# Optimization experiments

Hardware: AMD Instinct MI355X
Metric: run time of the kernel (lower is better)

Reference implementation:

```python
import jax, jax.numpy as jnp
import numpy as np

G, D, O, L, H, K, B = 33538, 256, 512, 6, 8, 2048, 4
FF = 4 * D
EPS = 1e-5
THRESH = 0.0


def _ln(x, s, b):
    mu = jnp.mean(x, axis=-1, keepdims=True)
    var = jnp.mean((x - mu) ** 2, axis=-1, keepdims=True)
    return (x - mu) * jax.lax.rsqrt(var + EPS) * s + b


def setup_inputs() -> dict:
    key = jax.random.key(0)
    ks = iter(jax.random.split(key, 32))
    s = 0.02
    rn = lambda shape, scale=s: jax.random.normal(next(ks), shape, dtype=jnp.float32) * scale
    inp = {
        'expr': jax.random.normal(next(ks), (B, G), dtype=jnp.float32),
        'gene_emb': rn((G, D)),
        'ep_w1': rn((D, 1), 0.5), 'ep_b1': jnp.zeros((D,), jnp.float32),
        'ep_w2': rn((D, D)), 'ep_b2': jnp.zeros((D,), jnp.float32),
        'cls': rn((D,), 1.0),
        'ln1_s': jnp.ones((L, D), jnp.float32), 'ln1_b': jnp.zeros((L, D), jnp.float32),
        'qkv_w': rn((L, 3 * D, D)), 'qkv_b': jnp.zeros((L, 3 * D), jnp.float32),
        'out_w': rn((L, D, D)), 'out_b': jnp.zeros((L, D), jnp.float32),
        'ln2_s': jnp.ones((L, D), jnp.float32), 'ln2_b': jnp.zeros((L, D), jnp.float32),
        'ff_w1': rn((L, FF, D)), 'ff_b1': jnp.zeros((L, FF), jnp.float32),
        'ff_w2': rn((L, D, FF)), 'ff_b2': jnp.zeros((L, D), jnp.float32),
        'fn_s': jnp.ones((D,), jnp.float32), 'fn_b': jnp.zeros((D,), jnp.float32),
        'pr_w1': rn((O, D)), 'pr_b1': jnp.zeros((O,), jnp.float32),
        'pr_w2': rn((O, O)), 'pr_b2': jnp.zeros((O,), jnp.float32),
    }
    return inp


def _encoder(expr, gene_emb, ep_w1, ep_b1, ep_w2, ep_b2, cls,
             ln1_s, ln1_b, qkv_w, qkv_b, out_w, out_b, ln2_s, ln2_b,
             ff_w1, ff_b1, ff_w2, ff_b2, fn_s, fn_b,
             pr_w1, pr_b1, pr_w2, pr_b2):
    Bb, Gg = expr.shape
    # --- tokeniser: token_i = gene_emb[i] + MLP(expr_i) for all genes ---
    h = jax.nn.gelu(expr[..., None] * ep_w1[:, 0] + ep_b1, approximate=False)  # [B,G,D]
    val_emb = jnp.einsum('bgd,ed->bge', h, ep_w2) + ep_b2
    tokens_all = gene_emb[None] + val_emb  # [B,G,D]
    # active-gene selection: threshold AND top-K
    active = expr > THRESH
    _, topk_idx = jax.lax.top_k(expr, K)
    sel = jnp.zeros((Bb, Gg), bool).at[jnp.arange(Bb)[:, None], topk_idx].set(True)
    active = active & sel
    counts = jnp.sum(active, axis=1)  # [B]
    # vectorized ragged packing: stable sort puts active genes (ascending id) first
    order = jnp.argsort(jnp.logical_not(active), axis=1, stable=True)[:, :K]  # [B,K]
    gathered = jnp.take_along_axis(tokens_all, order[..., None], axis=1)      # [B,K,D]
    valid = jnp.arange(K)[None, :] < counts[:, None]                          # [B,K]
    body = jnp.where(valid[..., None], gathered, 0.0)
    tokens = jnp.concatenate([jnp.broadcast_to(cls, (Bb, 1, D)), body], axis=1)  # [B,T,D]
    mask = jnp.concatenate([jnp.ones((Bb, 1), bool), valid], axis=1)             # [B,T]
    T = K + 1
    dh = D // H
    bias = jnp.where(mask, 0.0, -1e9)[:, None, None, :]  # key padding
    x = tokens
    for i in range(L):
        y = _ln(x, ln1_s[i], ln1_b[i])
        qkv = y @ qkv_w[i].T + qkv_b[i]
        q, k, v = jnp.split(qkv, 3, axis=-1)
        q = q.reshape(Bb, T, H, dh).transpose(0, 2, 1, 3)
        k = k.reshape(Bb, T, H, dh).transpose(0, 2, 1, 3)
        v = v.reshape(Bb, T, H, dh).transpose(0, 2, 1, 3)
        scores = jnp.einsum('bhqd,bhkd->bhqk', q, k) / np.sqrt(dh) + bias
        a = jax.nn.softmax(scores, axis=-1)
        o = jnp.einsum('bhqk,bhkd->bhqd', a, v).transpose(0, 2, 1, 3).reshape(Bb, T, D)
        x = x + o @ out_w[i].T + out_b[i]
        y2 = _ln(x, ln2_s[i], ln2_b[i])
        x = x + jax.nn.gelu(y2 @ ff_w1[i].T + ff_b1[i], approximate=False) @ ff_w2[i].T + ff_b2[i]
    x = _ln(x, fn_s, fn_b)
    cls_out = x[:, 0]
    return jax.nn.gelu(cls_out @ pr_w1.T + pr_b1, approximate=False) @ pr_w2.T + pr_b2


def reference(expr, gene_emb, ep_w1, ep_b1, ep_w2, ep_b2, cls,
              ln1_s, ln1_b, qkv_w, qkv_b, out_w, out_b, ln2_s, ln2_b,
              ff_w1, ff_b1, ff_w2, ff_b2, fn_s, fn_b,
              pr_w1, pr_b1, pr_w2, pr_b2):
    return _encoder(expr, gene_emb, ep_w1, ep_b1, ep_w2, ep_b2, cls,
                    ln1_s, ln1_b, qkv_w, qkv_b, out_w, out_b, ln2_s, ln2_b,
                    ff_w1, ff_b1, ff_w2, ff_b2, fn_s, fn_b,
                    pr_w1, pr_b1, pr_w2, pr_b2)
```

## Files before the change

### kernel.cpp

```cpp
#include <hip/hip_runtime.h>
#include <hip/hip_bf16.h>
#include <math.h>

#define GG 33538
#define DD 256
#define LL 6
#define HH 8
#define KK 2048
#define BB 4
#define TT 2049
#define BT (BB*TT)
#define NT 65
#define QSC (0.17677669529663688f * 1.44269504088896340f)

typedef __bf16 bf16x8 __attribute__((ext_vector_type(8)));
typedef float f32x4 __attribute__((ext_vector_type(4)));
typedef float f32x16 __attribute__((ext_vector_type(16)));
typedef unsigned short ub16;

union BW { __bf16 h; ub16 u; };
__device__ __forceinline__ ub16 f2b(float x) { BW w; w.h = (__bf16)x; return w.u; }
__device__ __forceinline__ unsigned pk2(float a, float b) {
    return (unsigned)f2b(a) | ((unsigned)f2b(b) << 16);
}
union U4B { unsigned u[4]; bf16x8 v; };

__device__ __forceinline__ float gelu_f(float x) {
    return 0.5f * x * (1.0f + erff(x * 0.70710678118654752440f));
}

__device__ __forceinline__ unsigned to_key(float x) {
    unsigned u = __float_as_uint(x);
    return (u & 0x80000000u) ? ~u : (u | 0x80000000u);
}

__device__ int block_scan_excl_1024(int v, int* shw) {
    int lane = threadIdx.x & 63, w = threadIdx.x >> 6;
    int x = v;
    #pragma unroll
    for (int o = 1; o < 64; o <<= 1) {
        int t = __shfl_up(x, o, 64);
        if (lane >= o) x += t;
    }
    if (lane == 63) shw[w] = x;
    __syncthreads();
    if (w == 0) {
        int y = (lane < 16) ? shw[lane] : 0;
        #pragma unroll
        for (int o = 1; o < 16; o <<= 1) {
            int t = __shfl_up(y, o, 64);
            if (lane >= o) y += t;
        }
        if (lane < 16) shw[lane] = y;
    }
    __syncthreads();
    int off = (w == 0) ? 0 : shw[w - 1];
    return off + x - v;
}

#define TKCH 33

__global__ __launch_bounds__(1024) void topk_kernel(const float* __restrict__ expr,
                                                    int* __restrict__ idxout,
                                                    int* __restrict__ cntout) {
    __shared__ unsigned hist[16][256];
    __shared__ int shw[16];
    __shared__ unsigned sh_prefix;
    __shared__ int sh_want;
    __shared__ int sh_tot2;

    int b = blockIdx.x;
    int tid = threadIdx.x, wv = tid >> 6;
    const float* row = expr + (size_t)b * GG;

    unsigned prefix = 0;
    int want = KK;
    for (int p = 3; p >= 0; --p) {
        for (int i = tid; i < 16 * 256; i += 1024) ((unsigned*)hist)[i] = 0u;
        __syncthreads();
        int shift = p * 8;
        unsigned pmask = (p == 3) ? 0u : (0xFFFFFFFFu << (shift + 8));
        for (int i = tid; i < GG / 4; i += 1024) {
            float4 v4 = *(const float4*)(row + 4 * i);
            float vv[4] = {v4.x, v4.y, v4.z, v4.w};
            #pragma unroll
            for (int j = 0; j < 4; ++j) {
                unsigned key = to_key(vv[j]);
                if ((key & pmask) == (prefix & pmask))
                    atomicAdd(&hist[wv][(key >> shift) & 255u], 1u);
            }
        }
        if (tid < 2) {
            unsigned key = to_key(row[33536 + tid]);
            if ((key & pmask) == (prefix & pmask))
                atomicAdd(&hist[15][(key >> shift) & 255u], 1u);
        }
        __syncthreads();
        unsigned cnt = 0;
        if (tid < 256) {
            #pragma unroll
            for (int j = 1; j < 16; ++j) cnt += hist[j][tid];
            cnt += hist[0][tid];
            hist[0][tid] = cnt;
        }
        __syncthreads();
        int v = (tid < 256) ? (int)hist[0][255 - tid] : 0;
        int above = block_scan_excl_1024(v, shw);
        if (tid < 256 && above < want && above + v >= want) {
            sh_prefix = prefix | ((unsigned)(255 - tid) << shift);
            sh_want = want - above;
        }
        __syncthreads();
        prefix = sh_prefix;
        want = sh_want;
        __syncthreads();
    }
    unsigned kth = prefix;

    int start = tid * TKCH;
    int end = min(start + TKCH, GG);
    int c_eq = 0;
    for (int g = start; g < end; ++g) c_eq += (to_key(row[g]) == kth);
    int eq_base = block_scan_excl_1024(c_eq, shw);

    int c_act = 0;
    {
        int leq = 0;
        for (int g = start; g < end; ++g) {
            float e = row[g];
            unsigned key = to_key(e);
            bool sel = (key > kth) || (key == kth && (eq_base + leq) < want);
            leq += (key == kth);
            c_act += (sel && e > 0.0f) ? 1 : 0;
        }
    }
    int out_base = block_scan_excl_1024(c_act, shw);
    if (tid == 1023) sh_tot2 = out_base + c_act;
    {
        int leq = 0, pos = out_base;
        for (int g = start; g < end; ++g) {
            float e = row[g];
            unsigned key = to_key(e);
            bool sel = (key > kth) || (key == kth && (eq_base + leq) < want);
            leq += (key == kth);
            if (sel && e > 0.0f) idxout[b * KK + pos++] = g;
        }
    }
    __syncthreads();
    if (tid == 0) cntout[b] = sh_tot2;
}

__global__ __launch_bounds__(256) void cvt_bf16_kernel(const float* __restrict__ s,
                                                       ub16* __restrict__ d, int n) {
    int i = blockIdx.x * 256 + threadIdx.x;
    if (i < n) d[i] = f2b(s[i]);
}

__global__ __launch_bounds__(256) void build_h_kernel(const float* __restrict__ expr,
                                                      const int* __restrict__ idxb,
                                                      const int* __restrict__ cntb,
                                                      const float* __restrict__ ep_w1,
                                                      const float* __restrict__ ep_b1,
                                                      ub16* __restrict__ H) {
    int i = blockIdx.x * 256 + threadIdx.x;
    int r = i >> 8, d = i & 255;
    int b = r >> 11, jj = r & (KK - 1);
    float v = 0.0f;
    if (jj < cntb[b]) {
        int g = idxb[b * KK + jj];
        float e = expr[(size_t)b * GG + g];
        v = gelu_f(e * ep_w1[d] + ep_b1[d]);
    }
    H[i] = f2b(v);
}

__global__ __launch_bounds__(256) void assemble_kernel(const float* __restrict__ VAL,
                                                       const float* __restrict__ gene_emb,
                                                       const float* __restrict__ clsv,
                                                       const int* __restrict__ idxb,
                                                       const int* __restrict__ cntb,
                                                       float* __restrict__ x) {
    int i = blockIdx.x * 256 + threadIdx.x;
    int r = i >> 8, d = i & 255;
    int b = r / TT, t = r % TT;
    float v;
    if (t == 0) {
        v = clsv[d];
    } else {
        int jj = t - 1;
        if (jj < cntb[b]) {
            int g = idxb[b * KK + jj];
            v = gene_emb[(size_t)g * DD + d] + VAL[((size_t)b * KK + jj) * DD + d];
        } else {
            v = 0.0f;
        }
    }
    x[i] = v;
}

__global__ __launch_bounds__(256) void ln_kernel(const float* __restrict__ X,
                                                 const float* __restrict__ s,
                                                 const float* __restrict__ bsh,
                                                 ub16* __restrict__ Y16,
                                                 float* __restrict__ Yf) {
    int w = threadIdx.x >> 6, lane = threadIdx.x & 63;
    size_t r = (size_t)blockIdx.x * 4 + w;
    float4 xv = *(const float4*)(X + r * 256 + lane * 4);
    float sum = xv.x + xv.y + xv.z + xv.w;
    #pragma unroll
    for (int o = 1; o < 64; o <<= 1) sum += __shfl_xor(sum, o);
    float mu = sum * (1.0f / 256.0f);
    float d0 = xv.x - mu, d1 = xv.y - mu, d2 = xv.z - mu, d3 = xv.w - mu;
    float vs = d0 * d0 + d1 * d1 + d2 * d2 + d3 * d3;
    #pragma unroll
    for (int o = 1; o < 64; o <<= 1) vs += __shfl_xor(vs, o);
    float rstd = rsqrtf(vs * (1.0f / 256.0f) + 1e-5f);
    float4 sc = *(const float4*)(s + lane * 4);
    float4 bc = *(const float4*)(bsh + lane * 4);
    float y0 = d0 * rstd * sc.x + bc.x;
    float y1 = d1 * rstd * sc.y + bc.y;
    float y2 = d2 * rstd * sc.z + bc.z;
    float y3 = d3 * rstd * sc.w + bc.w;
    if (Y16) {
        uint2 o2 = make_uint2(pk2(y0, y1), pk2(y2, y3));
        *(uint2*)(Y16 + r * 256 + lane * 4) = o2;
    } else {
        *(float4*)(Yf + r * 256 + lane * 4) = make_float4(y0, y1, y2, y3);
    }
}

__global__ __launch_bounds__(256) void gemm_bt16(const ub16* __restrict__ A,
                                                 const ub16* __restrict__ W,
                                                 const float* __restrict__ bias,
                                                 const float* __restrict__ R,
                                                 float* __restrict__ Cf,
                                                 ub16* __restrict__ Ch,
                                                 int M, int N, int K, int gelu_flag,
                                                 int qcols) {
    __shared__ ub16 As[2][64][40];
    __shared__ ub16 Ws[2][64][40];
    int tid = threadIdx.x;
    int lane = tid & 63, w = tid >> 6;
    int wr = (w >> 1) * 32, wc = (w & 1) * 32;
    int bm = blockIdx.y * 64, bn = blockIdx.x * 64;
    f32x4 acc[2][2] = {};

    int lrow = tid >> 2, lc8 = (tid & 3) * 8;
    int arow = min(bm + lrow, M - 1);
    const ub16* ap = A + (size_t)arow * K + lc8;
    const ub16* wp = W + (size_t)(bn + lrow) * K + lc8;

    int fr = lane & 15, fc = 8 * (lane >> 4);
    for (int k0 = 0; k0 < K; k0 += 64) {
        bf16x8 av0 = *(const bf16x8*)(ap + k0);
        bf16x8 av1 = *(const bf16x8*)(ap + k0 + 32);
        bf16x8 wv0 = *(const bf16x8*)(wp + k0);
        bf16x8 wv1 = *(const bf16x8*)(wp + k0 + 32);
        *(bf16x8*)&As[0][lrow][lc8] = av0;
        *(bf16x8*)&As[1][lrow][lc8] = av1;
        *(bf16x8*)&Ws[0][lrow][lc8] = wv0;
        *(bf16x8*)&Ws[1][lrow][lc8] = wv1;
        __syncthreads();
        #pragma unroll
        for (int ks = 0; ks < 2; ++ks) {
            bf16x8 a0 = *(const bf16x8*)&As[ks][wr + fr][fc];
            bf16x8 a1 = *(const bf16x8*)&As[ks][wr + 16 + fr][fc];
            bf16x8 b0 = *(const bf16x8*)&Ws[ks][wc + fr][fc];
            bf16x8 b1 = *(const bf16x8*)&Ws[ks][wc + 16 + fr][fc];
            acc[0][0] = __builtin_amdgcn_mfma_f32_16x16x32_bf16(a0, b0, acc[0][0], 0, 0, 0);
            acc[0][1] = __builtin_amdgcn_mfma_f32_16x16x32_bf16(a0, b1, acc[0][1], 0, 0, 0);
            acc[1][0] = __builtin_amdgcn_mfma_f32_16x16x32_bf16(a1, b0, acc[1][0], 0, 0, 0);
            acc[1][1] = __builtin_amdgcn_mfma_f32_16x16x32_bf16(a1, b1, acc[1][1], 0, 0, 0);
        }
        __syncthreads();
    }

    #pragma unroll
    for (int i = 0; i < 2; ++i) {
        #pragma unroll
        for (int j = 0; j < 2; ++j) {
            #pragma unroll
            for (int reg = 0; reg < 4; ++reg) {
                int gm = bm + wr + i * 16 + (lane >> 4) * 4 + reg;
                int gn = bn + wc + j * 16 + (lane & 15);
                if (gm >= M) continue;
                float v = acc[i][j][reg] + bias[gn];
                if (R) v += R[(size_t)gm * N + gn];
                if (gelu_flag) v = gelu_f(v);
                if (gn < qcols) v *= QSC;
                if (Cf) Cf[(size_t)gm * N + gn] = v;
                else    Ch[(size_t)gm * N + gn] = f2b(v);
            }
        }
    }
}

__global__ __launch_bounds__(256) void kvprep(const ub16* __restrict__ qkv,
                                              ub16* __restrict__ Kc,
                                              ub16* __restrict__ Vt) {
    __shared__ unsigned vl[32][33];
    int bh = blockIdx.x, b = bh >> 3, h = bh & 7;
    int c = blockIdx.y;
    int tid = threadIdx.x;
    int krel = tid >> 2;
    int key = c * 64 + krel;
    int d8 = (tid & 3) * 8;
    U4B kv = {}, vv = {};
    if (key < TT) {
        const ub16* p = qkv + ((size_t)(b * TT + key)) * 768 + 256 + h * 32 + d8;
        kv.v = *(const bf16x8*)p;
        vv.v = *(const bf16x8*)(p + 256);
    }
    int kt = c * 2 + (krel >> 5);
    if (kt < NT)
        *(bf16x8*)(Kc + (((size_t)bh * NT + kt) * 32 + (krel & 31)) * 32 + d8) = kv.v;

    unsigned pu[4];
    #pragma unroll
    for (int j = 0; j < 4; ++j) pu[j] = __shfl_xor(vv.u[j], 4);
    if (!(krel & 1)) {
        int kp = krel >> 1;
        #pragma unroll
        for (int j = 0; j < 8; ++j) {
            unsigned mine = (vv.u[j >> 1] >> ((j & 1) * 16)) & 0xffffu;
            unsigned oth  = (pu[j >> 1] >> ((j & 1) * 16)) & 0xffffu;
            vl[d8 + j][kp] = mine | (oth << 16);
        }
    }
    __syncthreads();
    int d = tid >> 3, c8 = tid & 7;
    int kt2 = c * 2 + (c8 >> 2);
    if (kt2 < NT) {
        unsigned* vdst = (unsigned*)(Vt + (((size_t)bh * NT + kt2) * 32 + d) * 32);
        #pragma unroll
        for (int ih = 0; ih < 2; ++ih) {
            int pkr = (c8 & 3) * 4 + ih * 2;
            int dp = (pkr & 1) | ((pkr & 2) << 1) | ((pkr & 4) >> 1) | (pkr & 8);
            uint2 o2 = make_uint2(vl[d][c8 * 4 + ih * 2], vl[d][c8 * 4 + ih * 2 + 1]);
            *(uint2*)(vdst + dp) = o2;
        }
    }
}

__global__ __launch_bounds__(256) void attn_mfma4(const ub16* __restrict__ qkv,
                                                  const ub16* __restrict__ Kc,
                                                  const ub16* __restrict__ Vt,
                                                  const int* __restrict__ cnt,
                                                  ub16* __restrict__ attno) {
    __shared__ float Olds[4][32][33];
    __shared__ float Oll[4][32];
    int bh = blockIdx.x, b = bh >> 3, h = bh & 7;
    int tid = threadIdx.x;
    int w = tid >> 6, lane = tid & 63, hi = lane >> 5, q = lane & 31;
    int qt = blockIdx.y;
    int t = qt * 32 + q;
    int nvalid = cnt[b] + 1;
    int nkt = (nvalid + 31) >> 5;
    int nfull = (nvalid & 31) ? nkt - 1 : nkt;

    int tc = min(t, TT - 1);
    const ub16* qp = qkv + ((size_t)(b * TT + tc)) * 768 + h * 32 + 8 * hi;
    bf16x8 bq0 = *(const bf16x8*)qp;
    bf16x8 bq1 = *(const bf16x8*)(qp + 16);

    float l = 0.0f;
    f32x16 ot = {};

    const ub16* kp = Kc + ((size_t)bh * NT + w) * 1024 + q * 32 + 8 * hi;
    const ub16* vp = Vt + ((size_t)bh * NT + w) * 1024 + q * 32 + 8 * hi;
    bf16x8 ka0 = *(const bf16x8*)kp;
    bf16x8 ka1 = *(const bf16x8*)(kp + 16);
    bf16x8 va0 = *(const bf16x8*)vp;
    bf16x8 va1 = *(const bf16x8*)(vp + 16);

    for (int kt = w; kt < nkt; kt += 4) {
        bf16x8 nk0 = ka0, nk1 = ka1, nv0 = va0, nv1 = va1;
        if (kt + 4 < nkt) {
            kp += 4096; vp += 4096;
            nk0 = *(const bf16x8*)kp;
            nk1 = *(const bf16x8*)(kp + 16);
            nv0 = *(const bf16x8*)vp;
            nv1 = *(const bf16x8*)(vp + 16);
        }
        f32x16 zz = {};
        f32x16 st = __builtin_amdgcn_mfma_f32_32x32x16_bf16(ka0, bq0, zz, 0, 0, 0);
        st = __builtin_amdgcn_mfma_f32_32x32x16_bf16(ka1, bq1, st, 0, 0, 0);

        if (kt >= nfull) {
            int k0 = kt << 5;
            #pragma unroll
            for (int r = 0; r < 16; ++r) {
                int key = k0 + (r & 3) + 8 * (r >> 2) + 4 * hi;
                if (key >= nvalid) st[r] = -1e30f;
            }
        }
        float tsum = 0.0f;
        #pragma unroll
        for (int r = 0; r < 16; ++r) {
            float p = exp2f(st[r]);
            st[r] = p;
            tsum += p;
        }
        tsum += __shfl_xor(tsum, 32);
        l += tsum;

        U4B p0, p1;
        #pragma unroll
        for (int jj = 0; jj < 4; ++jj) {
            p0.u[jj] = pk2(st[2 * jj], st[2 * jj + 1]);
            p1.u[jj] = pk2(st[8 + 2 * jj], st[9 + 2 * jj]);
        }
        ot = __builtin_amdgcn_mfma_f32_32x32x16_bf16(va0, p0.v, ot, 0, 0, 0);
        ot = __builtin_amdgcn_mfma_f32_32x32x16_bf16(va1, p1.v, ot, 0, 0, 0);

        ka0 = nk0; ka1 = nk1; va0 = nv0; va1 = nv1;
    }

    #pragma unroll
    for (int r = 0; r < 16; ++r) {
        int d = (r & 3) + 8 * (r >> 2) + 4 * hi;
        Olds[w][q][d] = ot[r];
    }
    if (hi == 0) Oll[w][q] = l;
    __syncthreads();

    int qq = tid >> 3, dg = tid & 7;
    int trow = qt * 32 + qq;
    if (trow < TT) {
        float L = Oll[0][qq] + Oll[1][qq] + Oll[2][qq] + Oll[3][qq];
        float rL = 1.0f / L;
        float o[4];
        #pragma unroll
        for (int j = 0; j < 4; ++j) {
            int d = dg * 4 + j;
            o[j] = (Olds[0][qq][d] + Olds[1][qq][d] +
                    Olds[2][qq][d] + Olds[3][qq][d]) * rL;
        }
        uint2 o2 = make_uint2(pk2(o[0], o[1]), pk2(o[2], o[3]));
        *(uint2*)(attno + ((size_t)(b * TT + trow)) * 256 + h * 32 + dg * 4) = o2;
    }
}

__global__ __launch_bounds__(512) void head_kernel(const float* __restrict__ Y,
                                                   const float* __restrict__ w1,
                                                   const float* __restrict__ b1,
                                                   const float* __restrict__ w2,
                                                   const float* __restrict__ b2,
                                                   float* __restrict__ out) {
    __shared__ float clsr[256];
    __shared__ float t1[512];
    int b = blockIdx.x, tid = threadIdx.x;
    if (tid < 256) clsr[tid] = Y[((size_t)b * TT) * DD + tid];
    __syncthreads();
    float acc = b1[tid];
    const float* w = w1 + (size_t)tid * 256;
    for (int k = 0; k < 256; ++k) acc += clsr[k] * w[k];
    t1[tid] = gelu_f(acc);
    __syncthreads();
    float acc2 = b2[tid];
    const float* wr = w2 + (size_t)tid * 512;
    for (int k = 0; k < 512; ++k) acc2 += t1[k] * wr[k];
    out[(size_t)b * 512 + tid] = acc2;
}

extern "C" void kernel_launch(void* const* d_in, const int* in_sizes, int n_in,
                              void* d_out, int out_size, void* d_ws, size_t ws_size,
                              hipStream_t stream) {
    (void)in_sizes; (void)n_in; (void)out_size; (void)ws_size;
    const float* expr     = (const float*)d_in[0];
    const float* gene_emb = (const float*)d_in[1];
    const float* ep_w1    = (const float*)d_in[2];
    const float* ep_b1    = (const float*)d_in[3];
    const float* ep_w2    = (const float*)d_in[4];
    const float* ep_b2    = (const float*)d_in[5];
    const float* clsv     = (const float*)d_in[6];
    const float* ln1_s    = (const float*)d_in[7];
    const float* ln1_b    = (const float*)d_in[8];
    const float* qkv_w    = (const float*)d_in[9];
    const float* qkv_b    = (const float*)d_in[10];
    const float* out_w    = (const float*)d_in[11];
    const float* out_b    = (const float*)d_in[12];
    const float* ln2_s    = (const float*)d_in[13];
    const float* ln2_b    = (const float*)d_in[14];
    const float* ff_w1    = (const float*)d_in[15];
    const float* ff_b1    = (const float*)d_in[16];
    const float* ff_w2    = (const float*)d_in[17];
    const float* ff_b2    = (const float*)d_in[18];
    const float* fn_s     = (const float*)d_in[19];
    const float* fn_b     = (const float*)d_in[20];
    const float* pr_w1    = (const float*)d_in[21];
    const float* pr_b1    = (const float*)d_in[22];
    const float* pr_w2    = (const float*)d_in[23];
    const float* pr_b2    = (const float*)d_in[24];
    float* outp = (float*)d_out;

    const size_t KVSZ = (size_t)32 * NT * 1024;

    float* x   = (float*)d_ws;
    float* VAL = x + (size_t)BT * 256;
    ub16* y16   = (ub16*)(VAL + (size_t)8192 * 256);
    ub16* qkv16 = y16 + (size_t)BT * 256;
    ub16* att16 = qkv16 + (size_t)BT * 768;
    ub16* ff116 = att16 + (size_t)BT * 256;
    ub16* kc_h  = ff116 + (size_t)BT * 1024;
    ub16* wqkv  = kc_h + KVSZ;
    ub16* wout  = wqkv + (size_t)LL * 768 * 256;
    ub16* wff1  = wout + (size_t)LL * 256 * 256;
    ub16* wff2  = wff1 + (size_t)LL * 1024 * 256;
    ub16* wep2  = wff2 + (size_t)LL * 256 * 1024;
    int*  idxb  = (int*)(wep2 + (size_t)256 * 256);
    int*  cntb  = idxb + BB * KK;
    ub16* H16 = kc_h;
    ub16* Kc  = kc_h;
    ub16* Vt  = (ub16*)VAL;

    topk_kernel<<<BB, 1024, 0, stream>>>(expr, idxb, cntb);

    cvt_bf16_kernel<<<(LL*768*256 + 255)/256, 256, 0, stream>>>(qkv_w, wqkv, LL*768*256);
    cvt_bf16_kernel<<<(LL*256*256 + 255)/256, 256, 0, stream>>>(out_w, wout, LL*256*256);
    cvt_bf16_kernel<<<(LL*1024*256 + 255)/256, 256, 0, stream>>>(ff_w1, wff1, LL*1024*256);
    cvt_bf16_kernel<<<(LL*256*1024 + 255)/256, 256, 0, stream>>>(ff_w2, wff2, LL*256*1024);
    cvt_bf16_kernel<<<(256*256 + 255)/256, 256, 0, stream>>>(ep_w2, wep2, 256*256);

    build_h_kernel<<<(BB * KK * DD) / 256, 256, 0, stream>>>(expr, idxb, cntb, ep_w1, ep_b1, H16);
    gemm_bt16<<<dim3(4, 128), 256, 0, stream>>>(H16, wep2, ep_b2, nullptr, VAL, nullptr,
                                                8192, 256, 256, 0, 0);
    assemble_kernel<<<BT, 256, 0, stream>>>(VAL, gene_emb, clsv, idxb, cntb, x);

    for (int i = 0; i < LL; ++i) {
        ln_kernel<<<BT / 4, 256, 0, stream>>>(x, ln1_s + i * DD, ln1_b + i * DD, y16, nullptr);
        gemm_bt16<<<dim3(12, 129), 256, 0, stream>>>(y16, wqkv + (size_t)i * 768 * 256,
                                                     qkv_b + i * 768, nullptr, nullptr, qkv16,
                                                     BT, 768, 256, 0, 256);
        kvprep<<<dim3(BB * HH, 33), 256, 0, stream>>>(qkv16, Kc, Vt);
        attn_mfma4<<<dim3(BB * HH, NT), 256, 0, stream>>>(qkv16, Kc, Vt, cntb, att16);
        gemm_bt16<<<dim3(4, 129), 256, 0, stream>>>(att16, wout + (size_t)i * 256 * 256,
                                                    out_b + i * 256, x, x, nullptr,
                                                    BT, 256, 256, 0, 0);
        ln_kernel<<<BT / 4, 256, 0, stream>>>(x, ln2_s + i * DD, ln2_b + i * DD, y16, nullptr);
        gemm_bt16<<<dim3(16, 129), 256, 0, stream>>>(y16, wff1 + (size_t)i * 1024 * 256,
                                                     ff_b1 + i * 1024, nullptr, nullptr, ff116,
                                                     BT, 1024, 256, 1, 0);
        gemm_bt16<<<dim3(4, 129), 256, 0, stream>>>(ff116, wff2 + (size_t)i * 256 * 1024,
                                                    ff_b2 + i * 256, x, x, nullptr,
                                                    BT, 256, 1024, 0, 0);
    }

    ln_kernel<<<BT / 4, 256, 0, stream>>>(x, fn_s, fn_b, nullptr, VAL);
    head_kernel<<<BB, 512, 0, stream>>>(VAL, pr_w1, pr_b1, pr_w2, pr_b2, outp);
}
```

Measured before the change: 1.014 ms.

## Parallelize top-k across blocks, add 64x128 GEMM tile, unroll attention two tiles

Three unrelated changes land together. The single-block-per-row radix top-k becomes a multi-kernel pipeline: global histograms per pass, a small select kernel, then count, scan and compact kernels spread over 7 blocks per row. A new 64x128 output-tile GEMM with register-prefetched double-buffered LDS handles the QKV and FF1 projections. The attention inner loop now processes two key tiles per iteration with separate accumulators, giving more independent MFMA work. The price is many more small kernel launches for top-k plus global atomics, and higher register pressure in attention.

```diff
diff --git a/kernel.cpp b/kernel.cpp
--- a/kernel.cpp
+++ b/kernel.cpp
@@ -11,6 +11,7 @@
 #define TT 2049
 #define BT (BB*TT)
 #define NT 65
+#define TCH 7
 #define QSC (0.17677669529663688f * 1.44269504088896340f)
 
 typedef __bf16 bf16x8 __attribute__((ext_vector_type(8)));
@@ -58,96 +59,178 @@
     return off + x - v;
 }
 
-#define TKCH 33
-
-__global__ __launch_bounds__(1024) void topk_kernel(const float* __restrict__ expr,
-                                                    int* __restrict__ idxout,
-                                                    int* __restrict__ cntout) {
-    __shared__ unsigned hist[16][256];
+__global__ void topk_init(unsigned* __restrict__ prefwant, unsigned* __restrict__ histg) {
+    int i = threadIdx.x;
+    if (i < BB * 256) histg[i] = 0u;
+    if (i < BB) { prefwant[2 * i] = 0u; prefwant[2 * i + 1] = KK; }
+}
+
+__global__ __launch_bounds__(1024) void topk_hist(const float* __restrict__ expr,
+                                                  const unsigned* __restrict__ prefwant,
+                                                  unsigned* __restrict__ histg, int pass) {
+    __shared__ unsigned lh[16][256];
+    int b = blockIdx.x, blk = blockIdx.y, tid = threadIdx.x, wv = tid >> 6;
+    for (int i = tid; i < 16 * 256; i += 1024) ((unsigned*)lh)[i] = 0u;
+    __syncthreads();
+    unsigned prefix = prefwant[2 * b];
+    int shift = pass * 8;
+    unsigned pmask = (pass == 3) ? 0u : (0xFFFFFFFFu << (shift + 8));
+    const float* row = expr + (size_t)b * GG;
+    int base = blk * 5120;
+    #pragma unroll
+    for (int j = 0; j < 5; ++j) {
+        int g = base + j * 1024 + tid;
+        if (g < GG) {
+            unsigned key = to_key(row[g]);
+            if ((key & pmask) == (prefix & pmask))
+                atomicAdd(&lh[wv][(key >> shift) & 255u], 1u);
+        }
+    }
+    __syncthreads();
+    if (tid < 256) {
+        unsigned s = 0;
+        #pragma unroll
+        for (int j = 0; j < 16; ++j) s += lh[j][tid];
+        if (s) atomicAdd(&histg[b * 256 + tid], s);
+    }
+}
+
+__global__ void topk_select(unsigned* __restrict__ prefwant,
+                            unsigned* __restrict__ histg, int pass) {
+    int b = blockIdx.x, lane = threadIdx.x;
+    int shift = pass * 8;
+    unsigned pref = prefwant[2 * b];
+    int want = (int)prefwant[2 * b + 1];
+    unsigned cc[4];
+    #pragma unroll
+    for (int j = 0; j < 4; ++j) cc[j] = histg[b * 256 + lane * 4 + j];
+    int s = (int)(cc[0] + cc[1] + cc[2] + cc[3]);
+    int incl = s;
+    #pragma unroll
+    for (int o = 1; o < 64; o <<= 1) { int t = __shfl_up(incl, o); if (lane >= o) incl += t; }
+    int total = __shfl(incl, 63);
+    int a3 = total - incl;
+    int a2 = a3 + (int)cc[3], a1 = a2 + (int)cc[2], a0 = a1 + (int)cc[1];
+    int av[4] = {a0, a1, a2, a3};
+    #pragma unroll
+    for (int j = 0; j < 4; ++j) {
+        if (av[j] < want && av[j] + (int)cc[j] >= want) {
+            prefwant[2 * b] = pref | ((unsigned)(lane * 4 + j) << shift);
+            prefwant[2 * b + 1] = (unsigned)(want - av[j]);
+        }
+    }
+    #pragma unroll
+    for (int j = 0; j < 4; ++j) histg[b * 256 + lane * 4 + j] = 0u;
+}
+
+__global__ __launch_bounds__(1024) void topk_c1(const float* __restrict__ expr,
+                                                const unsigned* __restrict__ prefwant,
+                                                int* __restrict__ blkcnt) {
+    __shared__ int sred[16][2];
+    int b = blockIdx.x, blk = blockIdx.y, tid = threadIdx.x;
+    unsigned kth = prefwant[2 * b];
+    const float* row = expr + (size_t)b * GG;
+    int start = blk * 5120 + tid * 5;
+    int eq = 0, gtp = 0;
+    #pragma unroll
+    for (int j = 0; j < 5; ++j) {
+        int g = start + j;
+        if (g < GG) {
+            float e = row[g];
+            unsigned key = to_key(e);
+            eq += (key == kth);
+            gtp += (key > kth && e > 0.0f);
+        }
+    }
+    #pragma unroll
+    for (int o = 1; o < 64; o <<= 1) { eq += __shfl_xor(eq, o); gtp += __shfl_xor(gtp, o); }
+    if ((tid & 63) == 0) { sred[tid >> 6][0] = eq; sred[tid >> 6][1] = gtp; }
+    __syncthreads();
+    if (tid == 0) {
+        int te = 0, tg = 0;
+        #pragma unroll
+        for (int i = 0; i < 16; ++i) { te += sred[i][0]; tg += sred[i][1]; }
+        blkcnt[(b * TCH + blk) * 2] = te;
+        blkcnt[(b * TCH + blk) * 2 + 1] = tg;
+    }
+}
+
+__global__ void topk_c2(const unsigned* __restrict__ prefwant,
+                        const int* __restrict__ blkcnt,
+                        int* __restrict__ blkbase, int* __restrict__ cntout) {
+    int b = blockIdx.x, lane = threadIdx.x;
+    int eq = 0, gtp = 0;
+    if (lane < TCH) {
+        eq = blkcnt[(b * TCH + lane) * 2];
+        gtp = blkcnt[(b * TCH + lane) * 2 + 1];
+    }
+    int want = (int)prefwant[2 * b + 1];
+    bool kthpos = prefwant[2 * b] > 0x80000000u;
+    int incl = eq;
+    #pragma unroll
+    for (int o = 1; o < 8; o <<= 1) { int t = __shfl_up(incl, o); if (lane >= o) incl += t; }
+    int eqb = incl - eq;
+    int eqsel = kthpos ? min(max(want - eqb, 0), eq) : 0;
+    int act = gtp + eqsel;
+    int incl2 = act;
+    #pragma unroll
+    for (int o = 1; o < 8; o <<= 1) { int t = __shfl_up(incl2, o); if (lane >= o) incl2 += t; }
+    int outb = incl2 - act;
+    if (lane < TCH) {
+        blkbase[(b * TCH + lane) * 2] = eqb;
+        blkbase[(b * TCH + lane) * 2 + 1] = outb;
+    }
+    if (lane == TCH - 1) cntout[b] = incl2;
+}
+
+__global__ __launch_bounds__(1024) void topk_c3(const float* __restrict__ expr,
+                                                const unsigned* __restrict__ prefwant,
+                                                const int* __restrict__ blkbase,
+                                                int* __restrict__ idxout) {
     __shared__ int shw[16];
-    __shared__ unsigned sh_prefix;
-    __shared__ int sh_want;
-    __shared__ int sh_tot2;
-
-    int b = blockIdx.x;
-    int tid = threadIdx.x, wv = tid >> 6;
+    int b = blockIdx.x, blk = blockIdx.y, tid = threadIdx.x;
+    unsigned kth = prefwant[2 * b];
+    int want = (int)prefwant[2 * b + 1];
     const float* row = expr + (size_t)b * GG;
-
-    unsigned prefix = 0;
-    int want = KK;
-    for (int p = 3; p >= 0; --p) {
-        for (int i = tid; i < 16 * 256; i += 1024) ((unsigned*)hist)[i] = 0u;
-        __syncthreads();
-        int shift = p * 8;
-        unsigned pmask = (p == 3) ? 0u : (0xFFFFFFFFu << (shift + 8));
-        for (int i = tid; i < GG / 4; i += 1024) {
-            float4 v4 = *(const float4*)(row + 4 * i);
-            float vv[4] = {v4.x, v4.y, v4.z, v4.w};
-            #pragma unroll
-            for (int j = 0; j < 4; ++j) {
-                unsigned key = to_key(vv[j]);
-                if ((key & pmask) == (prefix & pmask))
-                    atomicAdd(&hist[wv][(key >> shift) & 255u], 1u);
-            }
-        }
-        if (tid < 2) {
-            unsigned key = to_key(row[33536 + tid]);
-            if ((key & pmask) == (prefix & pmask))
-                atomicAdd(&hist[15][(key >> shift) & 255u], 1u);
-        }
-        __syncthreads();
-        unsigned cnt = 0;
-        if (tid < 256) {
-            #pragma unroll
-            for (int j = 1; j < 16; ++j) cnt += hist[j][tid];
-            cnt += hist[0][tid];
-            hist[0][tid] = cnt;
-        }
-        __syncthreads();
-        int v = (tid < 256) ? (int)hist[0][255 - tid] : 0;
-        int above = block_scan_excl_1024(v, shw);
-        if (tid < 256 && above < want && above + v >= want) {
-            sh_prefix = prefix | ((unsigned)(255 - tid) << shift);
-            sh_want = want - above;
-        }
-        __syncthreads();
-        prefix = sh_prefix;
-        want = sh_want;
-        __syncthreads();
-    }
-    unsigned kth = prefix;
-
-    int start = tid * TKCH;
-    int end = min(start + TKCH, GG);
-    int c_eq = 0;
-    for (int g = start; g < end; ++g) c_eq += (to_key(row[g]) == kth);
-    int eq_base = block_scan_excl_1024(c_eq, shw);
-
-    int c_act = 0;
+    int start = blk * 5120 + tid * 5;
+    int eqt = 0;
+    #pragma unroll
+    for (int j = 0; j < 5; ++j) {
+        int g = start + j;
+        if (g < GG) eqt += (to_key(row[g]) == kth);
+    }
+    int eqbase = blkbase[(b * TCH + blk) * 2] + block_scan_excl_1024(eqt, shw);
+    __syncthreads();
+    int actt = 0;
     {
         int leq = 0;
-        for (int g = start; g < end; ++g) {
-            float e = row[g];
-            unsigned key = to_key(e);
-            bool sel = (key > kth) || (key == kth && (eq_base + leq) < want);
-            leq += (key == kth);
-            c_act += (sel && e > 0.0f) ? 1 : 0;
-        }
-    }
-    int out_base = block_scan_excl_1024(c_act, shw);
-    if (tid == 1023) sh_tot2 = out_base + c_act;
+        #pragma unroll
+        for (int j = 0; j < 5; ++j) {
+            int g = start + j;
+            if (g < GG) {
+                float e = row[g];
+                unsigned key = to_key(e);
+                bool sel = (key > kth) || (key == kth && (eqbase + leq) < want);
+                leq += (key == kth);
+                actt += (sel && e > 0.0f) ? 1 : 0;
+            }
+        }
+    }
+    int pos = blkbase[(b * TCH + blk) * 2 + 1] + block_scan_excl_1024(actt, shw);
     {
-        int leq = 0, pos = out_base;
-        for (int g = start; g < end; ++g) {
-            float e = row[g];
-            unsigned key = to_key(e);
-            bool sel = (key > kth) || (key == kth && (eq_base + leq) < want);
-            leq += (key == kth);
-            if (sel && e > 0.0f) idxout[b * KK + pos++] = g;
-        }
-    }
-    __syncthreads();
-    if (tid == 0) cntout[b] = sh_tot2;
+        int leq = 0;
+        #pragma unroll
+        for (int j = 0; j < 5; ++j) {
+            int g = start + j;
+            if (g < GG) {
+                float e = row[g];
+                unsigned key = to_key(e);
+                bool sel = (key > kth) || (key == kth && (eqbase + leq) < want);
+                leq += (key == kth);
+                if (sel && e > 0.0f) idxout[b * KK + pos++] = g;
+            }
+        }
+    }
 }
 
 __global__ __launch_bounds__(256) void cvt_bf16_kernel(const float* __restrict__ s,
@@ -295,6 +378,85 @@
     }
 }
 
+__global__ __launch_bounds__(256) void gemm_bn128(const ub16* __restrict__ A,
+                                                  const ub16* __restrict__ W,
+                                                  const float* __restrict__ bias,
+                                                  ub16* __restrict__ Ch,
+                                                  int M, int N, int K, int gelu_flag,
+                                                  int qcols) {
+    __shared__ ub16 As[2][64][40];
+    __shared__ ub16 Ws[2][128][40];
+    int tid = threadIdx.x, lane = tid & 63, w = tid >> 6;
+    int wr = (w >> 1) * 32, wc = (w & 1) * 64;
+    int bm = blockIdx.y * 64, bn = blockIdx.x * 128;
+    f32x4 acc[2][4] = {};
+
+    int arow = tid >> 2, aseg = tid & 3, aks = aseg >> 1, aoff = (aseg & 1) * 16;
+    const ub16* apg = A + (size_t)min(bm + arow, M - 1) * K + aseg * 16;
+    int wrow = tid >> 1, wks = tid & 1;
+    const ub16* wpg = W + (size_t)(bn + wrow) * K + wks * 32;
+    int fr = lane & 15, fc = 8 * (lane >> 4);
+
+    bf16x8 ra0 = *(const bf16x8*)apg;
+    bf16x8 ra1 = *(const bf16x8*)(apg + 8);
+    bf16x8 rb0 = *(const bf16x8*)wpg;
+    bf16x8 rb1 = *(const bf16x8*)(wpg + 8);
+    bf16x8 rb2 = *(const bf16x8*)(wpg + 16);
+    bf16x8 rb3 = *(const bf16x8*)(wpg + 24);
+
+    for (int k0 = 0; k0 < K; k0 += 64) {
+        *(bf16x8*)&As[aks][arow][aoff] = ra0;
+        *(bf16x8*)&As[aks][arow][aoff + 8] = ra1;
+        *(bf16x8*)&Ws[wks][wrow][0]  = rb0;
+        *(bf16x8*)&Ws[wks][wrow][8]  = rb1;
+        *(bf16x8*)&Ws[wks][wrow][16] = rb2;
+        *(bf16x8*)&Ws[wks][wrow][24] = rb3;
+        __syncthreads();
+        if (k0 + 64 < K) {
+            ra0 = *(const bf16x8*)(apg + k0 + 64);
+            ra1 = *(const bf16x8*)(apg + k0 + 72);
+            rb0 = *(const bf16x8*)(wpg + k0 + 64);
+            rb1 = *(const bf16x8*)(wpg + k0 + 72);
+            rb2 = *(const bf16x8*)(wpg + k0 + 80);
+            rb3 = *(const bf16x8*)(wpg + k0 + 88);
+        }
+        #pragma unroll
+        for (int ks = 0; ks < 2; ++ks) {
+            bf16x8 af[2], bfv[4];
+            #pragma unroll
+            for (int mr = 0; mr < 2; ++mr)
+                af[mr] = *(const bf16x8*)&As[ks][wr + mr * 16 + fr][fc];
+            #pragma unroll
+            for (int nr = 0; nr < 4; ++nr)
+                bfv[nr] = *(const bf16x8*)&Ws[ks][wc + nr * 16 + fr][fc];
+            #pragma unroll
+            for (int mr = 0; mr < 2; ++mr)
+                #pragma unroll
+                for (int nr = 0; nr < 4; ++nr)
+                    acc[mr][nr] = __builtin_amdgcn_mfma_f32_16x16x32_bf16(
+                        af[mr], bfv[nr], acc[mr][nr], 0, 0, 0);
+        }
+        __syncthreads();
+    }
+
+    #pragma unroll
+    for (int mr = 0; mr < 2; ++mr) {
+        #pragma unroll
+        for (int nr = 0; nr < 4; ++nr) {
+            #pragma unroll
+            for (int reg = 0; reg < 4; ++reg) {
+                int gm = bm + wr + mr * 16 + (lane >> 4) * 4 + reg;
+                int gn = bn + wc + nr * 16 + (lane & 15);
+                if (gm >= M) continue;
+                float v = acc[mr][nr][reg] + bias[gn];
+                if (gelu_flag) v = gelu_f(v);
+                if (gn < qcols) v *= QSC;
+                Ch[(size_t)gm * N + gn] = f2b(v);
+            }
+        }
+    }
+}
+
 __global__ __launch_bounds__(256) void kvprep(const ub16* __restrict__ qkv,
                                               ub16* __restrict__ Kc,
                                               ub16* __restrict__ Vt) {
@@ -342,7 +504,7 @@
     }
 }
 
-__global__ __launch_bounds__(256) void attn_mfma4(const ub16* __restrict__ qkv,
+__global__ __launch_bounds__(256) void attn_mfma5(const ub16* __restrict__ qkv,
                                                   const ub16* __restrict__ Kc,
                                                   const ub16* __restrict__ Vt,
                                                   const int* __restrict__ cnt,
@@ -363,63 +525,87 @@
     bf16x8 bq0 = *(const bf16x8*)qp;
     bf16x8 bq1 = *(const bf16x8*)(qp + 16);
 
-    float l = 0.0f;
-    f32x16 ot = {};
-
-    const ub16* kp = Kc + ((size_t)bh * NT + w) * 1024 + q * 32 + 8 * hi;
-    const ub16* vp = Vt + ((size_t)bh * NT + w) * 1024 + q * 32 + 8 * hi;
-    bf16x8 ka0 = *(const bf16x8*)kp;
-    bf16x8 ka1 = *(const bf16x8*)(kp + 16);
-    bf16x8 va0 = *(const bf16x8*)vp;
-    bf16x8 va1 = *(const bf16x8*)(vp + 16);
-
-    for (int kt = w; kt < nkt; kt += 4) {
-        bf16x8 nk0 = ka0, nk1 = ka1, nv0 = va0, nv1 = va1;
-        if (kt + 4 < nkt) {
-            kp += 4096; vp += 4096;
-            nk0 = *(const bf16x8*)kp;
-            nk1 = *(const bf16x8*)(kp + 16);
-            nv0 = *(const bf16x8*)vp;
-            nv1 = *(const bf16x8*)(vp + 16);
-        }
-        f32x16 zz = {};
-        f32x16 st = __builtin_amdgcn_mfma_f32_32x32x16_bf16(ka0, bq0, zz, 0, 0, 0);
-        st = __builtin_amdgcn_mfma_f32_32x32x16_bf16(ka1, bq1, st, 0, 0, 0);
+    const ub16* kbase = Kc + (size_t)bh * NT * 1024 + q * 32 + 8 * hi;
+    const ub16* vbase = Vt + (size_t)bh * NT * 1024 + q * 32 + 8 * hi;
+
+    f32x16 ot0 = {}, ot1 = {};
+    float l0 = 0.0f, l1 = 0.0f;
+
+    size_t oA = (size_t)min(w, NT - 1) * 1024, oB = (size_t)min(w + 4, NT - 1) * 1024;
+    bf16x8 kA0 = *(const bf16x8*)(kbase + oA);
+    bf16x8 kA1 = *(const bf16x8*)(kbase + oA + 16);
+    bf16x8 vA0 = *(const bf16x8*)(vbase + oA);
+    bf16x8 vA1 = *(const bf16x8*)(vbase + oA + 16);
+    bf16x8 kB0 = *(const bf16x8*)(kbase + oB);
+    bf16x8 kB1 = *(const bf16x8*)(kbase + oB + 16);
+    bf16x8 vB0 = *(const bf16x8*)(vbase + oB);
+    bf16x8 vB1 = *(const bf16x8*)(vbase + oB + 16);
+
+    for (int kt = w; kt < nkt; kt += 8) {
+        size_t nA = (size_t)min(kt + 8, NT - 1) * 1024;
+        size_t nB = (size_t)min(kt + 12, NT - 1) * 1024;
+        bf16x8 nkA0 = *(const bf16x8*)(kbase + nA);
+        bf16x8 nkA1 = *(const bf16x8*)(kbase + nA + 16);
+        bf16x8 nvA0 = *(const bf16x8*)(vbase + nA);
+        bf16x8 nvA1 = *(const bf16x8*)(vbase + nA + 16);
+        bf16x8 nkB0 = *(const bf16x8*)(kbase + nB);
+        bf16x8 nkB1 = *(const bf16x8*)(kbase + nB + 16);
+        bf16x8 nvB0 = *(const bf16x8*)(vbase + nB);
+        bf16x8 nvB1 = *(const bf16x8*)(vbase + nB + 16);
+
+        f32x16 z = {};
+        f32x16 stA = __builtin_amdgcn_mfma_f32_32x32x16_bf16(kA0, bq0, z, 0, 0, 0);
+        stA = __builtin_amdgcn_mfma_f32_32x32x16_bf16(kA1, bq1, stA, 0, 0, 0);
+        f32x16 stB = __builtin_amdgcn_mfma_f32_32x32x16_bf16(kB0, bq0, z, 0, 0, 0);
+        stB = __builtin_amdgcn_mfma_f32_32x32x16_bf16(kB1, bq1, stB, 0, 0, 0);
 
         if (kt >= nfull) {
-            int k0 = kt << 5;
+            int lim = nvalid - (kt << 5);
             #pragma unroll
             for (int r = 0; r < 16; ++r) {
-                int key = k0 + (r & 3) + 8 * (r >> 2) + 4 * hi;
-                if (key >= nvalid) st[r] = -1e30f;
+                int off = (r & 3) + 8 * (r >> 2) + 4 * hi;
+                if (off >= lim) stA[r] = -1e30f;
             }
         }
-        float tsum = 0.0f;
-        #pragma unroll
-        for (int r = 0; r < 16; ++r) {
-            float p = exp2f(st[r]);
-            st[r] = p;
-            tsum += p;
-        }
-        tsum += __shfl_xor(tsum, 32);
-        l += tsum;
-
-        U4B p0, p1;
+        if (kt + 4 >= nfull) {
+            int lim = nvalid - ((kt + 4) << 5);
+            #pragma unroll
+            for (int r = 0; r < 16; ++r) {
+                int off = (r & 3) + 8 * (r >> 2) + 4 * hi;
+                if (off >= lim) stB[r] = -1e30f;
+            }
+        }
+
+        float tsA = 0.0f, tsB = 0.0f;
+        #pragma unroll
+        for (int r = 0; r < 16; ++r) { float p = exp2f(stA[r]); stA[r] = p; tsA += p; }
+        #pragma unroll
+        for (int r = 0; r < 16; ++r) { float p = exp2f(stB[r]); stB[r] = p; tsB += p; }
+        l0 += tsA; l1 += tsB;
+
+        U4B pA0, pA1, pB0, pB1;
         #pragma unroll
         for (int jj = 0; jj < 4; ++jj) {
-            p0.u[jj] = pk2(st[2 * jj], st[2 * jj + 1]);
-            p1.u[jj] = pk2(st[8 + 2 * jj], st[9 + 2 * jj]);
-        }
-        ot = __builtin_amdgcn_mfma_f32_32x32x16_bf16(va0, p0.v, ot, 0, 0, 0);
-        ot = __builtin_amdgcn_mfma_f32_32x32x16_bf16(va1, p1.v, ot, 0, 0, 0);
-
-        ka0 = nk0; ka1 = nk1; va0 = nv0; va1 = nv1;
-    }
-
+            pA0.u[jj] = pk2(stA[2 * jj], stA[2 * jj + 1]);
+            pA1.u[jj] = pk2(stA[8 + 2 * jj], stA[9 + 2 * jj]);
+            pB0.u[jj] = pk2(stB[2 * jj], stB[2 * jj + 1]);
+            pB1.u[jj] = pk2(stB[8 + 2 * jj], stB[9 + 2 * jj]);
+        }
+        ot0 = __builtin_amdgcn_mfma_f32_32x32x16_bf16(vA0, pA0.v, ot0, 0, 0, 0);
+        ot0 = __builtin_amdgcn_mfma_f32_32x32x16_bf16(vA1, pA1.v, ot0, 0, 0, 0);
+        ot1 = __builtin_amdgcn_mfma_f32_32x32x16_bf16(vB0, pB0.v, ot1, 0, 0, 0);
+        ot1 = __builtin_amdgcn_mfma_f32_32x32x16_bf16(vB1, pB1.v, ot1, 0, 0, 0);
+
+        kA0 = nkA0; kA1 = nkA1; vA0 = nvA0; vA1 = nvA1;
+        kB0 = nkB0; kB1 = nkB1; vB0 = nvB0; vB1 = nvB1;
+    }
+
+    float l = l0 + l1;
+    l += __shfl_xor(l, 32);
     #pragma unroll
     for (int r = 0; r < 16; ++r) {
         int d = (r & 3) + 8 * (r >> 2) + 4 * hi;
-        Olds[w][q][d] = ot[r];
+        Olds[w][q][d] = ot0[r] + ot1[r];
     }
     if (hi == 0) Oll[w][q] = l;
     __syncthreads();
@@ -510,11 +696,22 @@
     ub16* wep2  = wff2 + (size_t)LL * 256 * 1024;
     int*  idxb  = (int*)(wep2 + (size_t)256 * 256);
     int*  cntb  = idxb + BB * KK;
+    unsigned* prefwant = (unsigned*)(cntb + BB);
+    unsigned* histg    = prefwant + BB * 2;
+    int* blkcnt  = (int*)(histg + BB * 256);
+    int* blkbase = blkcnt + BB * TCH * 2;
     ub16* H16 = kc_h;
     ub16* Kc  = kc_h;
     ub16* Vt  = (ub16*)VAL;
 
-    topk_kernel<<<BB, 1024, 0, stream>>>(expr, idxb, cntb);
+    topk_init<<<1, 1024, 0, stream>>>(prefwant, histg);
+    for (int p = 3; p >= 0; --p) {
+        topk_hist<<<dim3(BB, TCH), 1024, 0, stream>>>(expr, prefwant, histg, p);
+        topk_select<<<BB, 64, 0, stream>>>(prefwant, histg, p);
+    }
+    topk_c1<<<dim3(BB, TCH), 1024, 0, stream>>>(expr, prefwant, blkcnt);
+    topk_c2<<<BB, 64, 0, stream>>>(prefwant, blkcnt, blkbase, cntb);
+    topk_c3<<<dim3(BB, TCH), 1024, 0, stream>>>(expr, prefwant, blkbase, idxb);
 
     cvt_bf16_kernel<<<(LL*768*256 + 255)/256, 256, 0, stream>>>(qkv_w, wqkv, LL*768*256);
     cvt_bf16_kernel<<<(LL*256*256 + 255)/256, 256, 0, stream>>>(out_w, wout, LL*256*256);
@@ -529,17 +726,17 @@
 
     for (int i = 0; i < LL; ++i) {
         ln_kernel<<<BT / 4, 256, 0, stream>>>(x, ln1_s + i * DD, ln1_b + i * DD, y16, nullptr);
-        gemm_bt16<<<dim3(12, 129), 256, 0, stream>>>(y16, wqkv + (size_t)i * 768 * 256,
-                                                     qkv_b + i * 768, nullptr, nullptr, qkv16,
+        gemm_bn128<<<dim3(6, 129), 256, 0, stream>>>(y16, wqkv + (size_t)i * 768 * 256,
+                                                     qkv_b + i * 768, qkv16,
                                                      BT, 768, 256, 0, 256);
         kvprep<<<dim3(BB * HH, 33), 256, 0, stream>>>(qkv16, Kc, Vt);
-        attn_mfma4<<<dim3(BB * HH, NT), 256, 0, stream>>>(qkv16, Kc, Vt, cntb, att16);
+        attn_mfma5<<<dim3(BB * HH, NT), 256, 0, stream>>>(qkv16, Kc, Vt, cntb, att16);
         gemm_bt16<<<dim3(4, 129), 256, 0, stream>>>(att16, wout + (size_t)i * 256 * 256,
                                                     out_b + i * 256, x, x, nullptr,
                                                     BT, 256, 256, 0, 0);
         ln_kernel<<<BT / 4, 256, 0, stream>>>(x, ln2_s + i * DD, ln2_b + i * DD, y16, nullptr);
-        gemm_bt16<<<dim3(16, 129), 256, 0, stream>>>(y16, wff1 + (size_t)i * 1024 * 256,
-                                                     ff_b1 + i * 1024, nullptr, nullptr, ff116,
+        gemm_bn128<<<dim3(8, 129), 256, 0, stream>>>(y16, wff1 + (size_t)i * 1024 * 256,
+                                                     ff_b1 + i * 1024, ff116,
                                                      BT, 1024, 256, 1, 0);
         gemm_bt16<<<dim3(4, 129), 256, 0, stream>>>(ff116, wff2 + (size_t)i * 256 * 1024,
                                                     ff_b2 + i * 256, x, x, nullptr,
```

Result: no change. 1.034 ms (+2.0%).
